# Optimization experiments

Measured on AMD Instinct MI355X. Metric: run time of the kernel, lower is better.

Reference implementation:

```python
import jax, jax.numpy as jnp
import numpy as np

IN_FEATURES = 256
OUT_FEATURES = 128
ALPHA = 0.2  # LeakyReLU negative slope
NEG_INF = -9e15
N_NODES = 8192


def _xavier_uniform(key, shape, gain):
    fan_in, fan_out = shape[0], shape[1]
    limit = gain * np.sqrt(6.0 / (fan_in + fan_out))
    return jax.random.uniform(key, shape, jnp.float32, -limit, limit)


def setup_inputs() -> dict:
    key = jax.random.key(0)
    k_h, k_adj, k_W, k_a = jax.random.split(key, 4)
    h = jax.random.normal(k_h, (N_NODES, IN_FEATURES), dtype=jnp.float32)
    adj = jax.random.randint(k_adj, (N_NODES, N_NODES), 0, 2, dtype=jnp.int32)
    W = _xavier_uniform(k_W, (IN_FEATURES, OUT_FEATURES), gain=1.414)
    a = _xavier_uniform(k_a, (2 * OUT_FEATURES, 1), gain=1.414)
    return {"h": h, "adj": adj, "W": W, "a": a}


def reference(h, adj, W, a):
    # Wh: (N, F_out)
    Wh = h @ W
    # Decompose a = [a1; a2]; e_ij = leakyrelu(Wh_i . a1 + Wh_j . a2)
    # == the original concat([Wh_i, Wh_j]) @ a, without the O(N^2*2F) tensor.
    a1 = a[:OUT_FEATURES, 0]  # (F_out,)
    a2 = a[OUT_FEATURES:, 0]  # (F_out,)
    src = Wh @ a1  # (N,)
    dst = Wh @ a2  # (N,)
    e = jax.nn.leaky_relu(src[:, None] + dst[None, :], negative_slope=ALPHA)  # (N, N)
    attention = jnp.where(adj > 0, e, NEG_INF)
    attention = jax.nn.softmax(attention, axis=1)
    # dropout p=0.0 (eval) -> identity
    h_prime = attention @ Wh  # (N, F_out)
    return jax.nn.elu(h_prime)  # concat=True
```

## Files before the change

kernel.cpp:

```cpp
#include <hip/hip_runtime.h>

#define N_NODES 8192
#define IN_F    256
#define OUT_F   128
#define ALPHA_S 0.2f

typedef __attribute__((ext_vector_type(8))) short  short8;
typedef __attribute__((ext_vector_type(4))) short  short4v;
typedef __attribute__((ext_vector_type(4))) float  floatx4;
typedef __attribute__((ext_vector_type(4))) int    intx4;
typedef __attribute__((ext_vector_type(4))) float  fx4;

static __device__ __forceinline__ short f2bf(float f) {
    union { float f; unsigned int i; } u; u.f = f;
    unsigned int r = u.i + 0x7FFFu + ((u.i >> 16) & 1u);
    return (short)(r >> 16);
}

__global__ __launch_bounds__(512) void k_wh(
    const float* __restrict__ h,
    const float* __restrict__ W,
    const float* __restrict__ a,
    short* __restrict__ WhB,
    float* __restrict__ src,
    float* __restrict__ dst)
{
    __shared__ short Wt[OUT_F][IN_F + 8];
    __shared__ short htile[32][IN_F + 8];
    __shared__ float q1s[IN_F], q2s[IN_F];
    __shared__ short wh_t[OUT_F][40];

    const int t      = threadIdx.x;
    const int lane   = t & 63;
    const int wave   = t >> 6;
    const int r_base = blockIdx.x * 32;

#pragma unroll
    for (int rep = 0; rep < 4; ++rep) {
        const int idx = rep * 8192 + t * 16;
        const int k   = idx >> 7;
        const int f   = idx & 127;
        fx4 w0 = *(const fx4*)(W + idx);
        fx4 w1 = *(const fx4*)(W + idx + 4);
        fx4 w2 = *(const fx4*)(W + idx + 8);
        fx4 w3 = *(const fx4*)(W + idx + 12);
        fx4 a10 = *(const fx4*)(a + f);
        fx4 a11 = *(const fx4*)(a + f + 4);
        fx4 a12 = *(const fx4*)(a + f + 8);
        fx4 a13 = *(const fx4*)(a + f + 12);
        fx4 a20 = *(const fx4*)(a + OUT_F + f);
        fx4 a21 = *(const fx4*)(a + OUT_F + f + 4);
        fx4 a22 = *(const fx4*)(a + OUT_F + f + 8);
        fx4 a23 = *(const fx4*)(a + OUT_F + f + 12);
        float p1 = 0.f, p2 = 0.f;
#pragma unroll
        for (int e = 0; e < 4; ++e) {
            p1 = fmaf(w0[e], a10[e], p1); p2 = fmaf(w0[e], a20[e], p2);
            p1 = fmaf(w1[e], a11[e], p1); p2 = fmaf(w1[e], a21[e], p2);
            p1 = fmaf(w2[e], a12[e], p1); p2 = fmaf(w2[e], a22[e], p2);
            p1 = fmaf(w3[e], a13[e], p1); p2 = fmaf(w3[e], a23[e], p2);
        }
#pragma unroll
        for (int e = 0; e < 4; ++e) {
            Wt[f + e][k]      = f2bf(w0[e]);
            Wt[f + 4 + e][k]  = f2bf(w1[e]);
            Wt[f + 8 + e][k]  = f2bf(w2[e]);
            Wt[f + 12 + e][k] = f2bf(w3[e]);
        }
#pragma unroll
        for (int m = 1; m < 8; m <<= 1) {
            p1 += __shfl_xor(p1, m, 64);
            p2 += __shfl_xor(p2, m, 64);
        }
        if ((t & 7) == 0) { q1s[k] = p1; q2s[k] = p2; }
    }

    const int r0   = t >> 4;
    const int fgrp = t & 15;
    const int k0   = fgrp * 16;
    fx4 h0, h1, h2, h3;
    {
        const float* hp = h + (size_t)(r_base + r0) * IN_F + k0;
        h0 = *(const fx4*)hp; h1 = *(const fx4*)(hp + 4);
        h2 = *(const fx4*)(hp + 8); h3 = *(const fx4*)(hp + 12);
        short8 b0, b1;
#pragma unroll
        for (int e = 0; e < 4; ++e) {
            b0[e]     = f2bf(h0[e]); b0[4 + e] = f2bf(h1[e]);
            b1[e]     = f2bf(h2[e]); b1[4 + e] = f2bf(h3[e]);
        }
        *(short8*)&htile[r0][k0]     = b0;
        *(short8*)&htile[r0][k0 + 8] = b1;
    }
    __syncthreads();

    {
        float sp = 0.f, dp = 0.f;
#pragma unroll
        for (int e = 0; e < 4; ++e) {
            sp = fmaf(h0[e], q1s[k0 + e], sp);      dp = fmaf(h0[e], q2s[k0 + e], dp);
            sp = fmaf(h1[e], q1s[k0 + 4 + e], sp);  dp = fmaf(h1[e], q2s[k0 + 4 + e], dp);
            sp = fmaf(h2[e], q1s[k0 + 8 + e], sp);  dp = fmaf(h2[e], q2s[k0 + 8 + e], dp);
            sp = fmaf(h3[e], q1s[k0 + 12 + e], sp); dp = fmaf(h3[e], q2s[k0 + 12 + e], dp);
        }
#pragma unroll
        for (int m = 1; m < 16; m <<= 1) {
            sp += __shfl_xor(sp, m, 64);
            dp += __shfl_xor(dp, m, 64);
        }
        if (fgrp == 0) { src[r_base + r0] = sp; dst[r_base + r0] = dp; }
    }

    const int ln15 = lane & 15;
    const int q    = lane >> 4;
    const int f0   = wave * 16;
    floatx4 c0 = {0.f, 0.f, 0.f, 0.f};
    floatx4 c1 = {0.f, 0.f, 0.f, 0.f};
#pragma unroll
    for (int s = 0; s < 8; ++s) {
        short8 bf  = *(const short8*)&Wt[f0 + ln15][s * 32 + q * 8];
        short8 a0f = *(const short8*)&htile[ln15][s * 32 + q * 8];
        short8 a1f = *(const short8*)&htile[16 + ln15][s * 32 + q * 8];
        c0 = __builtin_amdgcn_mfma_f32_16x16x32_bf16(a0f, bf, c0, 0, 0, 0);
        c1 = __builtin_amdgcn_mfma_f32_16x16x32_bf16(a1f, bf, c1, 0, 0, 0);
    }
    {
        short4v p0, p1;
#pragma unroll
        for (int r = 0; r < 4; ++r) { p0[r] = f2bf(c0[r]); p1[r] = f2bf(c1[r]); }
        *(short4v*)&wh_t[f0 + ln15][q * 4]      = p0;
        *(short4v*)&wh_t[f0 + ln15][16 + q * 4] = p1;
    }
    __syncthreads();
    {
        const int ft2 = t >> 6;
        const int l2  = t & 63;
        const int n2  = l2 & 15;
        const int q2  = l2 >> 4;
        short8 v = *(const short8*)&wh_t[ft2 * 16 + n2][q2 * 8];
        *(short8*)(WhB + (((size_t)blockIdx.x * 8 + ft2) * 64 + l2) * 8) = v;
    }
}

#define JSPLIT 8
#define JCH    (N_NODES / JSPLIT)
#define SJ     64
#define NSTEP  (JCH / SJ)

__global__ __launch_bounds__(256, 2) void k_attn(
    const int*   __restrict__ adj,
    const short* __restrict__ WhB,
    const float* __restrict__ src,
    const float* __restrict__ dstv,
    float* __restrict__ numer_part,
    float* __restrict__ denom_part)
{
    __shared__ float dlds[JCH];

    const int t    = threadIdx.x;
    const int lane = t & 63;
    const int wave = t >> 6;
    const int rg   = blockIdx.x >> 3;
    const int jc   = blockIdx.x & 7;
    const int r0w  = rg * 64 + wave * 16;
    const int jb   = jc * JCH;

    const int ln15 = lane & 15;
    const int q    = lane >> 4;

    *(fx4*)&dlds[t * 4] = *(const fx4*)(dstv + jb + t * 4);
    __syncthreads();

    const float srow = src[r0w + ln15];
    const int*   ab = adj + (size_t)(r0w + ln15) * N_NODES + jb + q * 8;
    const short* wb = WhB + (size_t)(jc * 32) * 4096 + lane * 8;

    floatx4 acc[8];
#pragma unroll
    for (int ft = 0; ft < 8; ++ft) acc[ft] = (floatx4){0.f, 0.f, 0.f, 0.f};
    floatx4 dacc = {0.f, 0.f, 0.f, 0.f};
    short8 ones;
#pragma unroll
    for (int j = 0; j < 8; ++j) ones[j] = (short)0x3F80;

    intx4  M0[4], M1[4];
    short8 B0[16], B1[16];

    auto loadstep = [&](int s, intx4* M, short8* B) {
        const int off = s * SJ;
        M[0] = *(const intx4*)(ab + off);
        M[1] = *(const intx4*)(ab + off + 4);
        M[2] = *(const intx4*)(ab + off + 32);
        M[3] = *(const intx4*)(ab + off + 36);
        const short* bs = wb + (size_t)(2 * s) * 4096;
#pragma unroll
        for (int ft = 0; ft < 8; ++ft) {
            B[2 * ft]     = *(const short8*)(bs + ft * 512);
            B[2 * ft + 1] = *(const short8*)(bs + 4096 + ft * 512);
        }
    };

    auto compute = [&](int s, const intx4* M, const short8* B) {
        const int off = s * SJ;
        fx4 d0 = *(const fx4*)&dlds[off + q * 8];
        fx4 d1 = *(const fx4*)&dlds[off + q * 8 + 4];
        fx4 d2 = *(const fx4*)&dlds[off + 32 + q * 8];
        fx4 d3 = *(const fx4*)&dlds[off + 32 + q * 8 + 4];
        short8 A0, A1;
#pragma unroll
        for (int e = 0; e < 4; ++e) {
            float x, l;
            x = srow + d0[e]; l = fmaxf(x, ALPHA_S * x);
            A0[e]     = (M[0][e] > 0) ? f2bf(__expf(l)) : (short)0;
            x = srow + d1[e]; l = fmaxf(x, ALPHA_S * x);
            A0[4 + e] = (M[1][e] > 0) ? f2bf(__expf(l)) : (short)0;
            x = srow + d2[e]; l = fmaxf(x, ALPHA_S * x);
            A1[e]     = (M[2][e] > 0) ? f2bf(__expf(l)) : (short)0;
            x = srow + d3[e]; l = fmaxf(x, ALPHA_S * x);
            A1[4 + e] = (M[3][e] > 0) ? f2bf(__expf(l)) : (short)0;
        }
        dacc = __builtin_amdgcn_mfma_f32_16x16x32_bf16(A0, ones, dacc, 0, 0, 0);
        dacc = __builtin_amdgcn_mfma_f32_16x16x32_bf16(A1, ones, dacc, 0, 0, 0);
#pragma unroll
        for (int ft = 0; ft < 8; ++ft) {
            acc[ft] = __builtin_amdgcn_mfma_f32_16x16x32_bf16(A0, B[2 * ft],     acc[ft], 0, 0, 0);
            acc[ft] = __builtin_amdgcn_mfma_f32_16x16x32_bf16(A1, B[2 * ft + 1], acc[ft], 0, 0, 0);
        }
    };

    loadstep(0, M0, B0);
    for (int s = 0; s < NSTEP; s += 2) {
        if (s + 1 < NSTEP) loadstep(s + 1, M1, B1);
        compute(s, M0, B0);
        if (s + 2 < NSTEP) loadstep(s + 2, M0, B0);
        if (s + 1 < NSTEP) compute(s + 1, M1, B1);
    }

    float* np = numer_part + ((size_t)jc * N_NODES + r0w) * OUT_F;
#pragma unroll
    for (int ft = 0; ft < 8; ++ft)
#pragma unroll
        for (int r = 0; r < 4; ++r)
            np[(size_t)(q * 4 + r) * OUT_F + ft * 16 + ln15] = acc[ft][r];
    if (ln15 == 0) {
        float* dp = denom_part + (size_t)jc * N_NODES + r0w;
#pragma unroll
        for (int r = 0; r < 4; ++r) dp[q * 4 + r] = dacc[r];
    }
}

__global__ void k_final(const float* __restrict__ numer_part,
                        const float* __restrict__ denom_part,
                        float* __restrict__ out) {
    const int idx = blockIdx.x * 256 + threadIdx.x;
    const int row = idx >> 7;
    float v = 0.f, dn = 0.f;
#pragma unroll
    for (int jc = 0; jc < JSPLIT; ++jc) {
        v  += numer_part[(size_t)jc * N_NODES * OUT_F + idx];
        dn += denom_part[(size_t)jc * N_NODES + row];
    }
    v = (dn != 0.f) ? (v / dn) : 0.f;
    v = v > 0.f ? v : (__expf(v) - 1.f);
    out[idx] = v;
}

extern "C" void kernel_launch(void* const* d_in, const int* in_sizes, int n_in,
                              void* d_out, int out_size, void* d_ws, size_t ws_size,
                              hipStream_t stream) {
    const float* h   = (const float*)d_in[0];
    const int*   adj = (const int*)d_in[1];
    const float* W   = (const float*)d_in[2];
    const float* a   = (const float*)d_in[3];
    float* out = (float*)d_out;

    char*  ws         = (char*)d_ws;
    float* denom_part = (float*)ws;
    short* WhB        = (short*)(ws + (256 << 10));
    float* src        = (float*)(ws + (256 << 10) + (2 << 20));
    float* dst        = src + N_NODES;
    float* numer_part = (float*)(ws + (4 << 20));

    k_wh   <<<256, 512, 0, stream>>>(h, W, a, WhB, src, dst);
    k_attn <<<1024, 256, 0, stream>>>(adj, WhB, src, dst, numer_part, denom_part);
    k_final<<<4096, 256, 0, stream>>>(numer_part, denom_part, out);
}
```

Before: 413.4 us.

## Split attention into weight materialization and a separate bf16 P·Wh GEMM

Replaces the fused attention kernel with two kernels. The first streams adj, computes the masked exp weights per row, writes them as a bf16 matrix P and reduces the row denominators. The second runs a tiled MFMA GEMM of P against Wh, staging P tiles in LDS. The aim is to decouple the element-wise exp/mask work from the matrix multiply so each runs near its own throughput limit, at the cost of an extra bf16 N×N round trip through memory and a larger workspace requirement.

```diff
diff --git a/kernel.cpp b/kernel.cpp
--- a/kernel.cpp
+++ b/kernel.cpp
@@ -11,6 +11,11 @@
 typedef __attribute__((ext_vector_type(4))) int    intx4;
 typedef __attribute__((ext_vector_type(4))) float  fx4;
 
+static __device__ __forceinline__ float bf2f(short s) {
+    union { unsigned int i; float f; } u;
+    u.i = ((unsigned int)(unsigned short)s) << 16;
+    return u.f;
+}
 static __device__ __forceinline__ short f2bf(float f) {
     union { float f; unsigned int i; } u; u.f = f;
     unsigned int r = u.i + 0x7FFFu + ((u.i >> 16) & 1u);
@@ -18,12 +23,9 @@
 }
 
 __global__ __launch_bounds__(512) void k_wh(
-    const float* __restrict__ h,
-    const float* __restrict__ W,
+    const float* __restrict__ h, const float* __restrict__ W,
     const float* __restrict__ a,
-    short* __restrict__ WhB,
-    float* __restrict__ src,
-    float* __restrict__ dst)
+    short* __restrict__ WhB, float* __restrict__ src, float* __restrict__ dst)
 {
     __shared__ short Wt[OUT_F][IN_F + 8];
     __shared__ short htile[32][IN_F + 8];
@@ -142,111 +144,119 @@
     }
 }
 
-#define JSPLIT 8
-#define JCH    (N_NODES / JSPLIT)
-#define SJ     64
-#define NSTEP  (JCH / SJ)
-
-__global__ __launch_bounds__(256, 2) void k_attn(
+__global__ __launch_bounds__(256) void k_weights(
     const int*   __restrict__ adj,
-    const short* __restrict__ WhB,
     const float* __restrict__ src,
     const float* __restrict__ dstv,
-    float* __restrict__ numer_part,
+    short* __restrict__ P,
     float* __restrict__ denom_part)
 {
-    __shared__ float dlds[JCH];
+    __shared__ float wsum[4];
+    const int bi  = blockIdx.x;
+    const int row = bi >> 1;
+    const int c0  = (bi & 1) * 4096;
+    const int t   = threadIdx.x;
+    const int col = c0 + t * 16;
+
+    const float srow = src[row];
+    const int*   ap = adj + (size_t)row * N_NODES + col;
+    const float* dp = dstv + col;
+
+    intx4 m[4]; fx4 d[4];
+#pragma unroll
+    for (int v = 0; v < 4; ++v) {
+        m[v] = *(const intx4*)(ap + v * 4);
+        d[v] = *(const fx4*)(dp + v * 4);
+    }
+
+    short8 w0, w1;
+    float lsum = 0.f;
+#pragma unroll
+    for (int v = 0; v < 4; ++v) {
+#pragma unroll
+        for (int e = 0; e < 4; ++e) {
+            float x = srow + d[v][e];
+            float l = fmaxf(x, ALPHA_S * x);
+            short b = (m[v][e] > 0) ? f2bf(__expf(l)) : (short)0;
+            lsum += bf2f(b);
+            if (v < 2) w0[v * 4 + e] = b;
+            else       w1[(v - 2) * 4 + e] = b;
+        }
+    }
+    short* pp = P + (size_t)row * N_NODES + col;
+    *(short8*)pp       = w0;
+    *(short8*)(pp + 8) = w1;
+
+#pragma unroll
+    for (int s = 1; s < 64; s <<= 1) lsum += __shfl_xor(lsum, s, 64);
+    if ((t & 63) == 0) wsum[t >> 6] = lsum;
+    __syncthreads();
+    if (t == 0)
+        denom_part[(size_t)(bi & 1) * N_NODES + row] =
+            wsum[0] + wsum[1] + wsum[2] + wsum[3];
+}
+
+#define KSPLIT 8
+#define KCH  (N_NODES / KSPLIT)
+#define PBK  128
+#define PSTR (PBK + 8)
+#define PNIT (KCH / PBK)
+
+__global__ __launch_bounds__(512) void k_pv(
+    const short* __restrict__ P,
+    const short* __restrict__ WhB,
+    float* __restrict__ numer_part)
+{
+    __shared__ short atile[128 * PSTR];
 
     const int t    = threadIdx.x;
     const int lane = t & 63;
     const int wave = t >> 6;
     const int rg   = blockIdx.x >> 3;
-    const int jc   = blockIdx.x & 7;
-    const int r0w  = rg * 64 + wave * 16;
-    const int jb   = jc * JCH;
+    const int kc   = blockIdx.x & 7;
+    const int r0   = rg * 128;
+    const int kb   = kc * KCH;
+    const int jb0  = kb >> 5;
 
     const int ln15 = lane & 15;
     const int q    = lane >> 4;
 
-    *(fx4*)&dlds[t * 4] = *(const fx4*)(dstv + jb + t * 4);
-    __syncthreads();
-
-    const float srow = src[r0w + ln15];
-    const int*   ab = adj + (size_t)(r0w + ln15) * N_NODES + jb + q * 8;
-    const short* wb = WhB + (size_t)(jc * 32) * 4096 + lane * 8;
+    const int srow2 = t >> 2;
+    const int sc    = (t & 3) * 32;
+    const short* pgl = P + (size_t)(r0 + srow2) * N_NODES + kb + sc;
+    short* lw = &atile[srow2 * PSTR + sc];
 
     floatx4 acc[8];
 #pragma unroll
-    for (int ft = 0; ft < 8; ++ft) acc[ft] = (floatx4){0.f, 0.f, 0.f, 0.f};
-    floatx4 dacc = {0.f, 0.f, 0.f, 0.f};
-    short8 ones;
-#pragma unroll
-    for (int j = 0; j < 8; ++j) ones[j] = (short)0x3F80;
-
-    intx4  M0[4], M1[4];
-    short8 B0[16], B1[16];
-
-    auto loadstep = [&](int s, intx4* M, short8* B) {
-        const int off = s * SJ;
-        M[0] = *(const intx4*)(ab + off);
-        M[1] = *(const intx4*)(ab + off + 4);
-        M[2] = *(const intx4*)(ab + off + 32);
-        M[3] = *(const intx4*)(ab + off + 36);
-        const short* bs = wb + (size_t)(2 * s) * 4096;
-#pragma unroll
-        for (int ft = 0; ft < 8; ++ft) {
-            B[2 * ft]     = *(const short8*)(bs + ft * 512);
-            B[2 * ft + 1] = *(const short8*)(bs + 4096 + ft * 512);
-        }
-    };
-
-    auto compute = [&](int s, const intx4* M, const short8* B) {
-        const int off = s * SJ;
-        fx4 d0 = *(const fx4*)&dlds[off + q * 8];
-        fx4 d1 = *(const fx4*)&dlds[off + q * 8 + 4];
-        fx4 d2 = *(const fx4*)&dlds[off + 32 + q * 8];
-        fx4 d3 = *(const fx4*)&dlds[off + 32 + q * 8 + 4];
-        short8 A0, A1;
-#pragma unroll
-        for (int e = 0; e < 4; ++e) {
-            float x, l;
-            x = srow + d0[e]; l = fmaxf(x, ALPHA_S * x);
-            A0[e]     = (M[0][e] > 0) ? f2bf(__expf(l)) : (short)0;
-            x = srow + d1[e]; l = fmaxf(x, ALPHA_S * x);
-            A0[4 + e] = (M[1][e] > 0) ? f2bf(__expf(l)) : (short)0;
-            x = srow + d2[e]; l = fmaxf(x, ALPHA_S * x);
-            A1[e]     = (M[2][e] > 0) ? f2bf(__expf(l)) : (short)0;
-            x = srow + d3[e]; l = fmaxf(x, ALPHA_S * x);
-            A1[4 + e] = (M[3][e] > 0) ? f2bf(__expf(l)) : (short)0;
-        }
-        dacc = __builtin_amdgcn_mfma_f32_16x16x32_bf16(A0, ones, dacc, 0, 0, 0);
-        dacc = __builtin_amdgcn_mfma_f32_16x16x32_bf16(A1, ones, dacc, 0, 0, 0);
-#pragma unroll
-        for (int ft = 0; ft < 8; ++ft) {
-            acc[ft] = __builtin_amdgcn_mfma_f32_16x16x32_bf16(A0, B[2 * ft],     acc[ft], 0, 0, 0);
-            acc[ft] = __builtin_amdgcn_mfma_f32_16x16x32_bf16(A1, B[2 * ft + 1], acc[ft], 0, 0, 0);
-        }
-    };
-
-    loadstep(0, M0, B0);
-    for (int s = 0; s < NSTEP; s += 2) {
-        if (s + 1 < NSTEP) loadstep(s + 1, M1, B1);
-        compute(s, M0, B0);
-        if (s + 2 < NSTEP) loadstep(s + 2, M0, B0);
-        if (s + 1 < NSTEP) compute(s + 1, M1, B1);
-    }
-
-    float* np = numer_part + ((size_t)jc * N_NODES + r0w) * OUT_F;
-#pragma unroll
-    for (int ft = 0; ft < 8; ++ft)
+    for (int rt = 0; rt < 8; ++rt) acc[rt] = (floatx4){0.f, 0.f, 0.f, 0.f};
+
+    for (int it = 0; it < PNIT; ++it) {
+        __syncthreads();
+        {
+            const short* pg = pgl + it * PBK;
+#pragma unroll
+            for (int u = 0; u < 4; ++u)
+                *(short8*)(lw + u * 8) = *(const short8*)(pg + u * 8);
+        }
+        __syncthreads();
+        const short* bbase = WhB + (((size_t)(jb0 + it * 4) * 8 + wave) * 64 + lane) * 8;
+#pragma unroll
+        for (int kf = 0; kf < 4; ++kf) {
+            short8 Bf = *(const short8*)(bbase + (size_t)kf * 8 * 64 * 8);
+#pragma unroll
+            for (int rt = 0; rt < 8; ++rt) {
+                short8 Af = *(const short8*)&atile[(rt * 16 + ln15) * PSTR + kf * 32 + q * 8];
+                acc[rt] = __builtin_amdgcn_mfma_f32_16x16x32_bf16(Af, Bf, acc[rt], 0, 0, 0);
+            }
+        }
+    }
+
+    float* np = numer_part + ((size_t)kc * N_NODES + r0) * OUT_F + wave * 16 + ln15;
+#pragma unroll
+    for (int rt = 0; rt < 8; ++rt)
 #pragma unroll
         for (int r = 0; r < 4; ++r)
-            np[(size_t)(q * 4 + r) * OUT_F + ft * 16 + ln15] = acc[ft][r];
-    if (ln15 == 0) {
-        float* dp = denom_part + (size_t)jc * N_NODES + r0w;
-#pragma unroll
-        for (int r = 0; r < 4; ++r) dp[q * 4 + r] = dacc[r];
-    }
+            np[(size_t)(rt * 16 + q * 4 + r) * OUT_F] = acc[rt][r];
 }
 
 __global__ void k_final(const float* __restrict__ numer_part,
@@ -254,12 +264,11 @@
                         float* __restrict__ out) {
     const int idx = blockIdx.x * 256 + threadIdx.x;
     const int row = idx >> 7;
-    float v = 0.f, dn = 0.f;
-#pragma unroll
-    for (int jc = 0; jc < JSPLIT; ++jc) {
-        v  += numer_part[(size_t)jc * N_NODES * OUT_F + idx];
-        dn += denom_part[(size_t)jc * N_NODES + row];
-    }
+    float v = 0.f;
+#pragma unroll
+    for (int kc = 0; kc < KSPLIT; ++kc)
+        v += numer_part[(size_t)kc * N_NODES * OUT_F + idx];
+    float dn = denom_part[row] + denom_part[N_NODES + row];
     v = (dn != 0.f) ? (v / dn) : 0.f;
     v = v > 0.f ? v : (__expf(v) - 1.f);
     out[idx] = v;
@@ -280,8 +289,10 @@
     float* src        = (float*)(ws + (256 << 10) + (2 << 20));
     float* dst        = src + N_NODES;
     float* numer_part = (float*)(ws + (4 << 20));
-
-    k_wh   <<<256, 512, 0, stream>>>(h, W, a, WhB, src, dst);
-    k_attn <<<1024, 256, 0, stream>>>(adj, WhB, src, dst, numer_part, denom_part);
-    k_final<<<4096, 256, 0, stream>>>(numer_part, denom_part, out);
-}
+    short* P          = (short*)(ws + (64ull << 20));
+
+    k_wh      <<<256, 512, 0, stream>>>(h, W, a, WhB, src, dst);
+    k_weights <<<16384, 256, 0, stream>>>(adj, src, dst, P, denom_part);
+    k_pv      <<<512, 512, 0, stream>>>(P, WhB, numer_part);
+    k_final   <<<4096, 256, 0, stream>>>(numer_part, denom_part, out);
+}
```

Result: slower. 441.9 us (+6.9%).
